# Performance work log

Hardware: AMD Instinct MI355X
Metric: run time of the kernel (lower is better)

The kernel has to match this reference:

```python
import jax, jax.numpy as jnp
import numpy as np

T_DIL = 10   # neighbor-count threshold
K_DIL = 2    # skip hyperparameter
BN_EPS = 1e-5
NORM_EPS = 1e-12


def _dilate_pattern(adj_bool, mask_b):
    """Sequential (row-by-row) dilated neighbor skipping on a [N,N] bool adjacency.
    Faithful to the torch double loop: earlier rows' removals (including the
    symmetric column zeroing) affect later rows' neighbor sets."""
    N = adj_bool.shape[0]

    def step(carry, n):
        row = jnp.take(carry, n, axis=0)                 # [N] bool, current neighbors of n
        nbi = row.astype(jnp.int32)
        num = jnp.sum(nbi)
        sf = jnp.where(num > T_DIL, (num + K_DIL - 1) // K_DIL, 1)  # linear mode, ceil(num/k)
        rank = jnp.cumsum(nbi)                           # 1-based rank among neighbors
        rm = row & ((rank % sf) == 0)                    # neighbors[sf-1::sf]
        valid = (mask_b[n] != 0) & (num > 1)
        rm = jnp.where(valid, rm, False)
        keep = ~rm
        carry = carry.at[n].set(row & keep)              # adj[n, to_remove] = 0
        carry = carry.at[:, n].set(carry[:, n] & keep)   # adj[to_remove, n] = 0
        return carry, None

    out, _ = jax.lax.scan(step, adj_bool, jnp.arange(N))
    return out


def _dilate(adj, mask):
    # keep-pattern is piecewise constant in adj; multiply so removed entries -> 0
    keep = jax.vmap(_dilate_pattern)(adj > 0, mask)
    return adj * keep.astype(adj.dtype)


def _sage(x, adj, Wr, Wx, b, mf):
    # DenseSAGEConv: mean-aggregate, lin_rel + lin_root, L2 normalize, mask
    deg = jnp.clip(jnp.sum(adj, axis=-1, keepdims=True), 1.0, None)
    agg = jnp.einsum('bij,bjd->bid', adj, x) / deg
    out = agg @ Wr + x @ Wx + b
    nrm = jnp.maximum(jnp.linalg.norm(out, axis=-1, keepdims=True), NORM_EPS)
    return (out / nrm) * mf[..., None]


def _bn(x, g, b):
    # BatchNorm1d in training mode over flattened (B*N) rows, biased variance
    m = jnp.mean(x, axis=(0, 1))
    v = jnp.var(x, axis=(0, 1))
    return (x - m) * jax.lax.rsqrt(v + BN_EPS) * g + b


def _forward(x, adj, mask, Wr1, Wx1, b1, g1, be1, Wr2, Wx2, b2, g2, be2,
             Wr3, Wx3, b3, g3, be3, Wl, bl):
    mf = mask.astype(x.dtype)
    # linear dilation mode: skip factor is layer-independent, and each layer
    # dilates the ORIGINAL adj (torch clones adj per call) -> compute once
    adj_d = _dilate(adj, mask)
    h1 = _bn(jax.nn.relu(_sage(x, adj_d, Wr1, Wx1, b1, mf)), g1, be1)
    h2 = _bn(jax.nn.relu(_sage(h1, adj_d, Wr2, Wx2, b2, mf)), g2, be2)
    h3 = _bn(jax.nn.relu(_sage(h2, adj_d, Wr3, Wx3, b3, mf)), g3, be3)
    xc = jnp.concatenate([h1, h2, h3], axis=-1) * mf[..., None]
    return (xc @ Wl + bl) * mf[..., None]


def setup_inputs() -> dict:
    B, N, D, H, E = 8, 2048, 128, 128, 128
    key = jax.random.key(0)
    ks = jax.random.split(key, 24)
    x = jax.random.normal(ks[0], (B, N, D), dtype=jnp.float32)
    a = jax.random.bernoulli(ks[1], 0.01, (B, N, N))
    a = a | jnp.swapaxes(a, 1, 2)
    a = a & ~jnp.eye(N, dtype=bool)[None]
    adj = a.astype(jnp.float32)
    mask = jnp.ones((B, N), dtype=jnp.int32)
    s = 0.05
    p = {}
    dims = [(D, H), (H, H), (H, E)]
    for i, (di, do) in enumerate(dims, 1):
        p[f'Wr{i}'] = s * jax.random.normal(ks[2 * i], (di, do), dtype=jnp.float32)
        p[f'Wx{i}'] = s * jax.random.normal(ks[2 * i + 1], (di, do), dtype=jnp.float32)
        p[f'b{i}'] = jnp.zeros((do,), dtype=jnp.float32)
        p[f'g{i}'] = jnp.ones((do,), dtype=jnp.float32)
        p[f'be{i}'] = jnp.zeros((do,), dtype=jnp.float32)
    p['Wl'] = s * jax.random.normal(ks[10], (2 * H + E, E), dtype=jnp.float32)
    p['bl'] = jnp.zeros((E,), dtype=jnp.float32)
    return {'x': x, 'adj': adj, 'mask': mask, **p}


def reference(x, adj, mask, Wr1, Wx1, b1, g1, be1, Wr2, Wx2, b2, g2, be2,
              Wr3, Wx3, b3, g3, be3, Wl, bl):
    return _forward(x, adj, mask, Wr1, Wx1, b1, g1, be1, Wr2, Wx2, b2, g2, be2,
                    Wr3, Wx3, b3, g3, be3, Wl, bl)
```

## Files before the change

kernel.cpp:

```cpp
#include <hip/hip_runtime.h>
#include <cstdint>

constexpr int B_ = 8, N_ = 2048, D_ = 128, NW = 64;
constexpr int EMAX = 131072;
constexpr int RPS = 2064;
constexpr int TDIL = 10;

constexpr size_t OFF_BITSET = 0;
constexpr size_t OFF_AGG    = 0;
constexpr size_t OFF_H1     = (size_t)8  << 20;
constexpr size_t OFF_H2     = (size_t)16 << 20;
constexpr size_t OFF_H3     = (size_t)24 << 20;
constexpr size_t OFF_XB     = (size_t)24 << 20;
constexpr size_t OFF_H1B    = (size_t)28 << 20;
constexpr size_t OFF_H2B    = (size_t)24 << 20;
constexpr size_t OFF_COLS   = (size_t)32 << 20;
constexpr size_t OFF_PACKED = (size_t)34 << 20;
constexpr size_t OFF_RP     = (size_t)38 << 20;
constexpr size_t OFF_DEG0   = OFF_RP   + ((size_t)128 << 10);
constexpr size_t OFF_DEGF   = OFF_DEG0 + ((size_t)64  << 10);
constexpr size_t OFF_RMASK  = OFF_DEGF + ((size_t)64  << 10);
constexpr size_t OFF_BN     = OFF_RMASK + ((size_t)256 << 10);
constexpr size_t OFF_WHI    = OFF_BN  + ((size_t)4 << 10);
constexpr size_t OFF_WLO    = OFF_WHI + ((size_t)304 << 10);

typedef __attribute__((ext_vector_type(8))) short short8v;
typedef __attribute__((ext_vector_type(4))) float f32x4;

__device__ __forceinline__ uint16_t bf16rne(float f) {
    uint32_t u = __float_as_uint(f);
    return (uint16_t)((u + 0x7FFFu + ((u >> 16) & 1u)) >> 16);
}

__global__ __launch_bounds__(256) void kW_prep(
        const float* __restrict__ Wr1, const float* __restrict__ Wx1,
        const float* __restrict__ Wr2, const float* __restrict__ Wx2,
        const float* __restrict__ Wr3, const float* __restrict__ Wx3,
        const float* __restrict__ Wl,
        uint16_t* __restrict__ whi, uint16_t* __restrict__ wlo,
        float* __restrict__ bn) {
    if (blockIdx.x == 0) {
        for (int i = threadIdx.x; i < 768; i += 256) bn[i] = 0.f;
    }
    int g  = blockIdx.x >> 5;
    int lb = blockIdx.x & 31;
    int K = (g == 3) ? 384 : 256;
    const float* A  = (g == 0) ? Wr1 : (g == 1) ? Wr2 : (g == 2) ? Wr3 : Wl;
    const float* Bw = (g == 0) ? Wx1 : (g == 1) ? Wx2 : (g == 2) ? Wx3 : nullptr;
    size_t base = (g == 3) ? (size_t)98304 : (size_t)g * 32768;
    int total = K * 128;
    for (int f = lb * 256 + threadIdx.x; f < total; f += 32 * 256) {
        int e = f & 7, lane = (f >> 3) & 63, ct = (f >> 9) & 7, ks = f >> 12;
        int k = ks * 32 + ((lane >> 4) << 3) + e;
        int col = (ct << 4) + (lane & 15);
        float v = (g == 3 || k < 128) ? A[(size_t)k * 128 + col]
                                      : Bw[(size_t)(k - 128) * 128 + col];
        uint32_t hi = bf16rne(v);
        float hf = __uint_as_float(hi << 16);
        whi[base + f] = (uint16_t)hi;
        wlo[base + f] = bf16rne(v - hf);
    }
}

__global__ __launch_bounds__(256) void kXB(const float* __restrict__ x,
                                           uint16_t* __restrict__ xb) {
    size_t i = ((size_t)blockIdx.x * 256 + threadIdx.x) * 4;
    float4 v = *(const float4*)&x[i];
    ushort4 o;
    o.x = bf16rne(v.x); o.y = bf16rne(v.y); o.z = bf16rne(v.z); o.w = bf16rne(v.w);
    *(ushort4*)&xb[i] = o;
}

__global__ __launch_bounds__(256) void k1_bitset(const float* __restrict__ adj,
        uint32_t* __restrict__ bitset, uint32_t* __restrict__ deg0) {
    int row  = blockIdx.x * 4 + (threadIdx.x >> 6);
    int lane = threadIdx.x & 63;
    const float* ar = adj + (size_t)row * N_;
    uint32_t myw = 0;
    #pragma unroll 4
    for (int it = 0; it < 32; ++it) {
        float v = ar[it * 64 + lane];
        unsigned long long m = __ballot(v != 0.0f);
        if (lane == 2 * it)          myw = (uint32_t)m;
        else if (lane == 2 * it + 1) myw = (uint32_t)(m >> 32);
    }
    bitset[(size_t)row * NW + lane] = myw;
    int pc = __popc(myw);
    #pragma unroll
    for (int off = 32; off >= 1; off >>= 1) pc += __shfl_xor(pc, off);
    if (lane == 0) deg0[row] = (uint32_t)pc;
}

__global__ __launch_bounds__(256) void k2_rowptr(const uint32_t* __restrict__ deg0,
        uint32_t* __restrict__ rowptr) {
    int b = blockIdx.x, t = threadIdx.x;
    __shared__ uint32_t tsum[256];
    uint32_t v[8]; uint32_t s = 0;
    #pragma unroll
    for (int j = 0; j < 8; ++j) { v[j] = deg0[b * N_ + t * 8 + j]; s += v[j]; v[j] = s; }
    tsum[t] = s;
    __syncthreads();
    for (int off = 1; off < 256; off <<= 1) {
        uint32_t xv = (t >= off) ? tsum[t - off] : 0u;
        __syncthreads();
        tsum[t] += xv;
        __syncthreads();
    }
    uint32_t excl = tsum[t] - s;
    uint32_t* rp = rowptr + (size_t)b * RPS;
    if (t == 0) rp[0] = 0;
    #pragma unroll
    for (int j = 0; j < 8; ++j) {
        uint32_t val = excl + v[j];
        if (val > (uint32_t)EMAX) val = EMAX;
        rp[t * 8 + j + 1] = val;
    }
}

__global__ __launch_bounds__(256) void k3_cols(const uint32_t* __restrict__ bitset,
        const uint32_t* __restrict__ rowptr, uint16_t* __restrict__ cols) {
    int row  = blockIdx.x * 4 + (threadIdx.x >> 6);
    int lane = threadIdx.x & 63;
    int b = row >> 11, n = row & (N_ - 1);
    uint32_t w = bitset[(size_t)row * NW + lane];
    uint32_t pc = __popc(w);
    uint32_t inc = pc;
    #pragma unroll
    for (int off = 1; off < 64; off <<= 1) {
        uint32_t t = __shfl_up(inc, off);
        if (lane >= off) inc += t;
    }
    uint32_t base = rowptr[(size_t)b * RPS + n] + (inc - pc);
    uint16_t* cb = cols + (size_t)b * EMAX;
    while (w) {
        int bit = __builtin_ctz(w); w &= w - 1;
        if (base < (uint32_t)EMAX) cb[base] = (uint16_t)(lane * 32 + bit);
        ++base;
    }
}

__global__ __launch_bounds__(256) void k4_packed(const uint16_t* __restrict__ cols,
        const uint32_t* __restrict__ rowptr, uint32_t* __restrict__ packed) {
    int row  = blockIdx.x * 4 + (threadIdx.x >> 6);
    int lane = threadIdx.x & 63;
    int b = row >> 11, n = row & (N_ - 1);
    const uint32_t* rpb = rowptr + (size_t)b * RPS;
    const uint16_t* cb  = cols + (size_t)b * EMAX;
    uint32_t start = rpb[n], end = rpb[n + 1];
    for (uint32_t e = start + lane; e < end; e += 64) {
        uint32_t j = cb[e];
        uint32_t lo = rpb[j], hi = rpb[j + 1];
        uint32_t rj = lo;
        while (lo < hi) {
            uint32_t mid = (lo + hi) >> 1;
            if ((int)cb[mid] < n) lo = mid + 1; else hi = mid;
        }
        packed[(size_t)b * EMAX + e] = j | ((lo - rj) << 16);
    }
}

#define K5_ISSUE(PK0, PK1, CNT, ROW)                                        \
    do {                                                                    \
        int rr_ = (ROW);                                                    \
        if (rr_ < N_) {                                                     \
            uint32_t ldI_ = rps[rr_], enI_ = rps[rr_ + 1];                  \
            CNT = (int)(enI_ - ldI_);                                       \
            PK0 = (lane < CNT)      ? pkg[ldI_ + lane]      : 0xFFFFFFFFu;  \
            PK1 = (lane + 64 < CNT) ? pkg[ldI_ + 64 + lane] : 0xFFFFFFFFu;  \
        } else { CNT = 0; PK0 = 0xFFFFFFFFu; PK1 = 0xFFFFFFFFu; }           \
    } while (0)

#define K5_PROC(PK0, PK1, CNT, NROW)                                        \
    do {                                                                    \
        int nr_ = (NROW);                                                   \
        uint32_t c0_ = PK0 & 0xFFFFu, c1_ = PK1 & 0xFFFFu;                  \
        bool e0_ = (lane < CNT)      && (c0_ < (uint32_t)nr_);              \
        bool e1_ = (lane + 64 < CNT) && (c1_ < (uint32_t)nr_);              \
        while (true) {                                                      \
            uint32_t d0_ = e0_ ? __hip_atomic_load(&done[c0_ >> 5],         \
                    __ATOMIC_ACQUIRE, __HIP_MEMORY_SCOPE_WORKGROUP) : 0u;   \
            uint32_t d1_ = e1_ ? __hip_atomic_load(&done[c1_ >> 5],         \
                    __ATOMIC_ACQUIRE, __HIP_MEMORY_SCOPE_WORKGROUP) : 0u;   \
            bool ok0_ = !e0_ || ((d0_ >> (c0_ & 31)) & 1u);                 \
            bool ok1_ = !e1_ || ((d1_ >> (c1_ & 31)) & 1u);                 \
            if (__all((int)(ok0_ && ok1_))) break;                          \
        }                                                                   \
        __builtin_amdgcn_s_setprio(1);                                      \
        uint4 mcur_ = *(const uint4*)&rm4[(size_t)nr_ * 4];                 \
        uint32_t w01_ = (lane < 32) ? mcur_.x : mcur_.y;                    \
        uint32_t w23_ = (lane < 32) ? mcur_.z : mcur_.w;                    \
        uint32_t a0_ = (w01_ >> (lane & 31)) & 1u;                          \
        uint32_t a1_ = (w23_ >> (lane & 31)) & 1u;                          \
        unsigned long long bl0_ = __ballot(a0_ != 0), bl1_ = __ballot(a1_ != 0); \
        uint32_t num_ = (uint32_t)__popcll(bl0_) + (uint32_t)__popcll(bl1_);\
        if (mk[nr_] && num_ > 1u) {                                         \
            bool allrm_ = num_ <= (uint32_t)TDIL;                           \
            uint32_t sf_ = (num_ + 1u) >> 1;                                \
            uint32_t r2_ = (num_ & 1u) ? 0xFFFFFFFFu : num_;                \
            uint32_t rank0_ = (uint32_t)__popcll(bl0_ & below) + 1u;        \
            uint32_t rank1_ = (uint32_t)__popcll(bl0_) +                    \
                              (uint32_t)__popcll(bl1_ & below) + 1u;        \
            bool rm0_ = a0_ && (allrm_ || rank0_ == sf_ || rank0_ == r2_);  \
            bool rm1_ = a1_ && (allrm_ || rank1_ == sf_ || rank1_ == r2_);  \
            unsigned long long rb0_ = __ballot(rm0_), rb1_ = __ballot(rm1_);\
            if (rm0_) {                                                     \
                uint32_t c_ = PK0 & 0xFFFFu, ml_ = PK0 >> 16;               \
                if (ml_ < 128u) atomicAnd(&rm4[c_ * 4 + (ml_ >> 5)], ~(1u << (ml_ & 31))); \
            }                                                               \
            if (rm1_) {                                                     \
                uint32_t c_ = PK1 & 0xFFFFu, ml_ = PK1 >> 16;               \
                if (ml_ < 128u) atomicAnd(&rm4[c_ * 4 + (ml_ >> 5)], ~(1u << (ml_ & 31))); \
            }                                                               \
            if (lane == 0) {                                                \
                uint4 nm_;                                                  \
                nm_.x = mcur_.x & ~(uint32_t)rb0_;                          \
                nm_.y = mcur_.y & ~(uint32_t)(rb0_ >> 32);                  \
                nm_.z = mcur_.z & ~(uint32_t)rb1_;                          \
                nm_.w = mcur_.w & ~(uint32_t)(rb1_ >> 32);                  \
                *(uint4*)&rm4[(size_t)nr_ * 4] = nm_;                       \
            }                                                               \
        }                                                                   \
        __asm__ __volatile__("" ::: "memory");                              \
        if (lane == 0)                                                      \
            __hip_atomic_fetch_or(&done[nr_ >> 5], 1u << (nr_ & 31),        \
                    __ATOMIC_RELAXED, __HIP_MEMORY_SCOPE_WORKGROUP);        \
        __builtin_amdgcn_s_setprio(0);                                      \
    } while (0)

__global__ __launch_bounds__(1024) void k5_dilate(
        const uint32_t* __restrict__ packed, const uint32_t* __restrict__ rowptr,
        const uint32_t* __restrict__ deg0, const int* __restrict__ mask,
        uint32_t* __restrict__ rmaskg, uint32_t* __restrict__ degf) {
    int b = blockIdx.x;
    int tid = threadIdx.x;
    int lane = tid & 63;
    int wv = tid >> 6;
    __shared__ __align__(16) uint32_t rm4[N_ * 4];
    __shared__ uint32_t rps[N_ + 1];
    __shared__ uint8_t  mk[N_];
    __shared__ uint32_t done[64];
    const uint32_t* pkg = packed + (size_t)b * EMAX;
    const uint32_t* rpg = rowptr + (size_t)b * RPS;

    for (int i = tid; i <= N_; i += 1024) rps[i] = rpg[i];
    if (tid < 64) done[tid] = 0u;
    for (int i = tid; i < N_; i += 1024) {
        int d = (int)deg0[b * N_ + i]; if (d > 128) d = 128;
        uint4 mm;
        mm.x = (d >= 32) ? ~0u : ((d > 0)  ? ((1u << d)        - 1u) : 0u);
        mm.y = (d >= 64) ? ~0u : ((d > 32) ? ((1u << (d - 32)) - 1u) : 0u);
        mm.z = (d >= 96) ? ~0u : ((d > 64) ? ((1u << (d - 64)) - 1u) : 0u);
        mm.w = (d >= 128)? ~0u : ((d > 96) ? ((1u << (d - 96)) - 1u) : 0u);
        *(uint4*)&rm4[(size_t)i * 4] = mm;
        mk[i] = (uint8_t)(mask[b * N_ + i] != 0);
    }
    __syncthreads();

    unsigned long long below = (1ULL << lane) - 1ULL;
    int cntA, cntB, cntC;
    uint32_t pkA0, pkA1, pkB0, pkB1, pkC0, pkC1;
    K5_ISSUE(pkA0, pkA1, cntA, wv);
    K5_ISSUE(pkB0, pkB1, cntB, wv + 16);
    K5_ISSUE(pkC0, pkC1, cntC, wv + 32);

    int n = wv;
    while (n < N_) {
        K5_PROC(pkA0, pkA1, cntA, n);
        K5_ISSUE(pkA0, pkA1, cntA, n + 48);
        n += 16; if (n >= N_) break;
        K5_PROC(pkB0, pkB1, cntB, n);
        K5_ISSUE(pkB0, pkB1, cntB, n + 48);
        n += 16; if (n >= N_) break;
        K5_PROC(pkC0, pkC1, cntC, n);
        K5_ISSUE(pkC0, pkC1, cntC, n + 48);
        n += 16;
    }
    __syncthreads();
    for (int i = tid; i < N_; i += 1024) {
        uint4 mm = *(const uint4*)&rm4[(size_t)i * 4];
        *(uint4*)&rmaskg[((size_t)b * N_ + i) * 4] = mm;
        degf[b * N_ + i] = (uint32_t)(__popc(mm.x) + __popc(mm.y) + __popc(mm.z) + __popc(mm.w));
    }
}

__global__ __launch_bounds__(256) void k6_compact(uint16_t* __restrict__ cols,
        const uint32_t* __restrict__ rowptr, const uint32_t* __restrict__ rmaskg) {
    int row  = blockIdx.x * 4 + (threadIdx.x >> 6);
    int lane = threadIdx.x & 63;
    int b = row >> 11, n = row & (N_ - 1);
    uint16_t* cb = cols + (size_t)b * EMAX;
    uint4 mm = *(const uint4*)&rmaskg[(size_t)row * 4];
    uint32_t st = rowptr[(size_t)b * RPS + n];
    uint32_t w01 = (lane < 32) ? mm.x : mm.y;
    uint32_t w23 = (lane < 32) ? mm.z : mm.w;
    uint32_t a0 = (w01 >> (lane & 31)) & 1u;
    uint32_t a1 = (w23 >> (lane & 31)) & 1u;
    unsigned long long b0 = __ballot(a0 != 0), b1 = __ballot(a1 != 0);
    unsigned long long below = (1ULL << lane) - 1ULL;
    uint16_t c0v = 0, c1v = 0;
    if (a0) c0v = cb[st + lane];
    if (a1) c1v = cb[st + 64 + lane];
    uint32_t i0 = st + (uint32_t)__popcll(b0 & below);
    uint32_t i1 = st + (uint32_t)__popcll(b0) + (uint32_t)__popcll(b1 & below);
    if (a0) cb[i0] = c0v;
    if (a1) cb[i1] = c1v;
}

__global__ __launch_bounds__(256) void k7_spmm(const uint16_t* __restrict__ Xb16,
        const uint16_t* __restrict__ cols, const uint32_t* __restrict__ rowptr,
        const uint32_t* __restrict__ degf, float* __restrict__ agg) {
    int wid  = blockIdx.x * 4 + (threadIdx.x >> 6);
    int lane = threadIdx.x & 63;
    int b = wid >> 11, n = wid & (N_ - 1);
    const uint16_t* cb = cols + (size_t)b * EMAX;
    uint32_t start = rowptr[(size_t)b * RPS + n];
    uint32_t cnt = degf[wid];
    const uint16_t* Xb = Xb16 + ((size_t)b * N_) * D_;
    float ax = 0.f, ay = 0.f;
    for (uint32_t base = 0; base < cnt; base += 64) {
        int idx = (int)base + lane;
        int cl = (idx < (int)cnt) ? (int)cb[start + idx] : 0;
        int kmax = (int)cnt - (int)base; if (kmax > 64) kmax = 64;
        int k = 0;
        for (; k + 4 <= kmax; k += 4) {
            int cA = __shfl(cl, k),     cB = __shfl(cl, k + 1);
            int cC = __shfl(cl, k + 2), cD = __shfl(cl, k + 3);
            uint32_t uA = ((const uint32_t*)(Xb + (size_t)cA * D_))[lane];
            uint32_t uB = ((const uint32_t*)(Xb + (size_t)cB * D_))[lane];
            uint32_t uC = ((const uint32_t*)(Xb + (size_t)cC * D_))[lane];
            uint32_t uD = ((const uint32_t*)(Xb + (size_t)cD * D_))[lane];
            ax += __uint_as_float(uA << 16) + __uint_as_float(uB << 16)
                + __uint_as_float(uC << 16) + __uint_as_float(uD << 16);
            ay += __uint_as_float(uA & 0xFFFF0000u) + __uint_as_float(uB & 0xFFFF0000u)
                + __uint_as_float(uC & 0xFFFF0000u) + __uint_as_float(uD & 0xFFFF0000u);
        }
        for (; k < kmax; ++k) {
            int c = __shfl(cl, k);
            uint32_t u = ((const uint32_t*)(Xb + (size_t)c * D_))[lane];
            ax += __uint_as_float(u << 16);
            ay += __uint_as_float(u & 0xFFFF0000u);
        }
    }
    float inv = 1.0f / (float)(cnt ? cnt : 1u);
    ((float2*)(agg + (size_t)wid * D_))[lane] = make_float2(ax * inv, ay * inv);
}

__device__ __forceinline__ void cvt_store4(uint16_t* hiA, uint16_t* loA,
                                           int idx, float4 v) {
    float vv[4] = {v.x, v.y, v.z, v.w};
    ushort4 hs, ls;
    uint16_t* hp = (uint16_t*)&hs; uint16_t* lp = (uint16_t*)&ls;
    #pragma unroll
    for (int i = 0; i < 4; ++i) {
        uint32_t hi = bf16rne(vv[i]);
        float hf = __uint_as_float(hi << 16);
        hp[i] = (uint16_t)hi;
        lp[i] = bf16rne(vv[i] - hf);
    }
    *(ushort4*)&hiA[idx] = hs;
    *(ushort4*)&loA[idx] = ls;
}

constexpr int ASTR = 264;
__global__ __launch_bounds__(256) void k8_mfma(const float* __restrict__ agg,
        const float* __restrict__ Hin,
        const uint16_t* __restrict__ whi, const uint16_t* __restrict__ wlo,
        const float* __restrict__ bias, const int* __restrict__ mask,
        const float* __restrict__ bnp, const float* __restrict__ gp,
        const float* __restrict__ bep, int use_bn,
        float* __restrict__ P, uint16_t* __restrict__ Pb,
        float* __restrict__ bnstat) {
    __shared__ __align__(16) char buf[2 * 32 * ASTR * 2];
    __shared__ float scL[128], shL[128];
    uint16_t* aHi = (uint16_t*)buf;
    uint16_t* aLo = (uint16_t*)(buf + 32 * ASTR * 2);
    float* outP = (float*)buf;
    int tid = threadIdx.x, lane = tid & 63, h = tid >> 6;
    size_t row0 = (size_t)blockIdx.x * 32;

    if (tid < 128) {
        float sc = 1.f, sh = 0.f;
        if (use_bn) {
            float mean = bnp[tid] * (1.f / 16384.f);
            float var  = bnp[128 + tid] * (1.f / 16384.f) - mean * mean;
            sc = gp[tid] * rsqrtf(var + 1e-5f);
            sh = bep[tid] - mean * sc;
        }
        scL[tid] = sc; shL[tid] = sh;
    }
    __syncthreads();

    for (int f = tid * 4; f < 4096; f += 1024) {
        int r = f >> 7, c = f & 127;
        float4 va = *(const float4*)&agg[(row0 + r) * 128 + c];
        float4 vx = *(const float4*)&Hin[(row0 + r) * 128 + c];
        float4 s4 = *(const float4*)&scL[c];
        float4 h4 = *(const float4*)&shL[c];
        va.x = va.x * s4.x + h4.x; va.y = va.y * s4.y + h4.y;
        va.z = va.z * s4.z + h4.z; va.w = va.w * s4.w + h4.w;
        vx.x = vx.x * s4.x + h4.x; vx.y = vx.y * s4.y + h4.y;
        vx.z = vx.z * s4.z + h4.z; vx.w = vx.w * s4.w + h4.w;
        cvt_store4(aHi, aLo, r * ASTR + c, va);
        cvt_store4(aHi, aLo, r * ASTR + 128 + c, vx);
    }
    __syncthreads();

    f32x4 acc00 = {0.f,0.f,0.f,0.f}, acc01 = acc00, acc10 = acc00, acc11 = acc00;
    int ct0 = h * 2, ct1 = h * 2 + 1;
    int arow = (lane & 15);
    int koff = (lane >> 4) * 8;
    #pragma unroll
    for (int ks = 0; ks < 8; ++ks) {
        int k0 = ks * 32 + koff;
        short8v a0h = *(short8v*)&aHi[arow * ASTR + k0];
        short8v a0l = *(short8v*)&aLo[arow * ASTR + k0];
        short8v a1h = *(short8v*)&aHi[(arow + 16) * ASTR + k0];
        short8v a1l = *(short8v*)&aLo[(arow + 16) * ASTR + k0];
        short8v b0h = *(const short8v*)&whi[(size_t)(((ks * 8 + ct0) << 6) + lane) * 8];
        short8v b0l = *(const short8v*)&wlo[(size_t)(((ks * 8 + ct0) << 6) + lane) * 8];
        short8v b1h = *(const short8v*)&whi[(size_t)(((ks * 8 + ct1) << 6) + lane) * 8];
        short8v b1l = *(const short8v*)&wlo[(size_t)(((ks * 8 + ct1) << 6) + lane) * 8];
        acc00 = __builtin_amdgcn_mfma_f32_16x16x32_bf16(a0h, b0h, acc00, 0, 0, 0);
        acc00 = __builtin_amdgcn_mfma_f32_16x16x32_bf16(a0h, b0l, acc00, 0, 0, 0);
        acc00 = __builtin_amdgcn_mfma_f32_16x16x32_bf16(a0l, b0h, acc00, 0, 0, 0);
        acc01 = __builtin_amdgcn_mfma_f32_16x16x32_bf16(a0h, b1h, acc01, 0, 0, 0);
        acc01 = __builtin_amdgcn_mfma_f32_16x16x32_bf16(a0h, b1l, acc01, 0, 0, 0);
        acc01 = __builtin_amdgcn_mfma_f32_16x16x32_bf16(a0l, b1h, acc01, 0, 0, 0);
        acc10 = __builtin_amdgcn_mfma_f32_16x16x32_bf16(a1h, b0h, acc10, 0, 0, 0);
        acc10 = __builtin_amdgcn_mfma_f32_16x16x32_bf16(a1h, b0l, acc10, 0, 0, 0);
        acc10 = __builtin_amdgcn_mfma_f32_16x16x32_bf16(a1l, b0h, acc10, 0, 0, 0);
        acc11 = __builtin_amdgcn_mfma_f32_16x16x32_bf16(a1h, b1h, acc11, 0, 0, 0);
        acc11 = __builtin_amdgcn_mfma_f32_16x16x32_bf16(a1h, b1l, acc11, 0, 0, 0);
        acc11 = __builtin_amdgcn_mfma_f32_16x16x32_bf16(a1l, b1h, acc11, 0, 0, 0);
    }
    __syncthreads();

    int orow = (lane >> 4) * 4;
    int oc0 = ct0 * 16 + (lane & 15);
    int oc1 = ct1 * 16 + (lane & 15);
    #pragma unroll
    for (int j = 0; j < 4; ++j) {
        outP[(orow + j) * 128 + oc0]      = acc00[j];
        outP[(orow + j) * 128 + oc1]      = acc01[j];
        outP[(16 + orow + j) * 128 + oc0] = acc10[j];
        outP[(16 + orow + j) * 128 + oc1] = acc11[j];
    }
    __syncthreads();

    float bs0 = bias[lane], bs1 = bias[lane + 64];
    #pragma unroll
    for (int i = 0; i < 8; ++i) {
        int r = h * 8 + i;
        float v0 = outP[r * 128 + lane] + bs0;
        float v1 = outP[r * 128 + lane + 64] + bs1;
        float s = v0 * v0 + v1 * v1;
        #pragma unroll
        for (int off = 32; off >= 1; off >>= 1) s += __shfl_xor(s, off);
        float nrm = fmaxf(sqrtf(s), 1e-12f);
        float mf = (mask[row0 + r] != 0) ? 1.f : 0.f;
        float inv = mf / nrm;
        float p0 = fmaxf(v0 * inv, 0.f), p1 = fmaxf(v1 * inv, 0.f);
        P[(row0 + r) * 128 + lane]      = p0;
        P[(row0 + r) * 128 + lane + 64] = p1;
        if (Pb) {
            Pb[(row0 + r) * 128 + lane]      = bf16rne(p0);
            Pb[(row0 + r) * 128 + lane + 64] = bf16rne(p1);
        }
        outP[r * 128 + lane] = p0; outP[r * 128 + lane + 64] = p1;
    }
    __syncthreads();
    if (tid < 128) {
        float s = 0.f, q = 0.f;
        #pragma unroll
        for (int r = 0; r < 32; ++r) { float v = outP[r * 128 + tid]; s += v; q += v * v; }
        atomicAdd(&bnstat[tid], s);
        atomicAdd(&bnstat[128 + tid], q);
    }
}

__global__ __launch_bounds__(256) void k11_final(const float* __restrict__ h1,
        const float* __restrict__ h2, const float* __restrict__ h3,
        const float* __restrict__ Wl, const float* __restrict__ bl,
        const int* __restrict__ mask, const float* __restrict__ bn,
        const float* __restrict__ g1, const float* __restrict__ be1,
        const float* __restrict__ g2, const float* __restrict__ be2,
        const float* __restrict__ g3, const float* __restrict__ be3,
        float* __restrict__ out) {
    __shared__ float s1[32 * 128], s2[32 * 128], s3[32 * 128];
    __shared__ float scA[128], shA[128], scB[128], shB[128], scC[128], shC[128];
    int tid = threadIdx.x;
    size_t row0 = (size_t)blockIdx.x * 32;
    if (tid < 128) {
        float m1 = bn[tid] * (1.f / 16384.f);
        float v1 = bn[128 + tid] * (1.f / 16384.f) - m1 * m1;
        scA[tid] = g1[tid] * rsqrtf(v1 + 1e-5f);
        shA[tid] = be1[tid] - m1 * scA[tid];
        float m2 = bn[256 + tid] * (1.f / 16384.f);
        float v2 = bn[384 + tid] * (1.f / 16384.f) - m2 * m2;
        scB[tid] = g2[tid] * rsqrtf(v2 + 1e-5f);
        shB[tid] = be2[tid] - m2 * scB[tid];
        float m3 = bn[512 + tid] * (1.f / 16384.f);
        float v3 = bn[640 + tid] * (1.f / 16384.f) - m3 * m3;
        scC[tid] = g3[tid] * rsqrtf(v3 + 1e-5f);
        shC[tid] = be3[tid] - m3 * scC[tid];
    }
    __syncthreads();
    for (int t = tid * 4; t < 32 * 128; t += 1024) {
        int r = t >> 7;
        float mf = (mask[row0 + r] != 0) ? 1.f : 0.f;
        int c = t & 127;
        float4 a = *(const float4*)&h1[row0 * 128 + t];
        float4 b = *(const float4*)&h2[row0 * 128 + t];
        float4 cc = *(const float4*)&h3[row0 * 128 + t];
        float4 sa = *(const float4*)&scA[c], ha = *(const float4*)&shA[c];
        float4 sb = *(const float4*)&scB[c], hb = *(const float4*)&shB[c];
        float4 sc = *(const float4*)&scC[c], hc = *(const float4*)&shC[c];
        a.x = (a.x * sa.x + ha.x) * mf; a.y = (a.y * sa.y + ha.y) * mf;
        a.z = (a.z * sa.z + ha.z) * mf; a.w = (a.w * sa.w + ha.w) * mf;
        b.x = (b.x * sb.x + hb.x) * mf; b.y = (b.y * sb.y + hb.y) * mf;
        b.z = (b.z * sb.z + hb.z) * mf; b.w = (b.w * sb.w + hb.w) * mf;
        cc.x = (cc.x * sc.x + hc.x) * mf; cc.y = (cc.y * sc.y + hc.y) * mf;
        cc.z = (cc.z * sc.z + hc.z) * mf; cc.w = (cc.w * sc.w + hc.w) * mf;
        *(float4*)&s1[t] = a; *(float4*)&s2[t] = b; *(float4*)&s3[t] = cc;
    }
    __syncthreads();
    int h = tid >> 6, c0 = (tid & 63) * 2;
    float2 acc[8];
    #pragma unroll
    for (int i = 0; i < 8; ++i) acc[i] = make_float2(0.f, 0.f);
    for (int k4 = 0; k4 < 128; k4 += 4) {
        float2 w1[4], w2[4], w3[4];
        #pragma unroll
        for (int kk = 0; kk < 4; ++kk) {
            w1[kk] = *(const float2*)&Wl[(k4 + kk) * 128 + c0];
            w2[kk] = *(const float2*)&Wl[(128 + k4 + kk) * 128 + c0];
            w3[kk] = *(const float2*)&Wl[(256 + k4 + kk) * 128 + c0];
        }
        #pragma unroll
        for (int i = 0; i < 8; ++i) {
            int r = h * 8 + i;
            float4 a = *(const float4*)&s1[r * 128 + k4];
            float4 b = *(const float4*)&s2[r * 128 + k4];
            float4 c = *(const float4*)&s3[r * 128 + k4];
            acc[i].x += a.x * w1[0].x + a.y * w1[1].x + a.z * w1[2].x + a.w * w1[3].x
                      + b.x * w2[0].x + b.y * w2[1].x + b.z * w2[2].x + b.w * w2[3].x
                      + c.x * w3[0].x + c.y * w3[1].x + c.z * w3[2].x + c.w * w3[3].x;
            acc[i].y += a.x * w1[0].y + a.y * w1[1].y + a.z * w1[2].y + a.w * w1[3].y
                      + b.x * w2[0].y + b.y * w2[1].y + b.z * w2[2].y + b.w * w2[3].y
                      + c.x * w3[0].y + c.y * w3[1].y + c.z * w3[2].y + c.w * w3[3].y;
        }
    }
    float bx = bl[c0], by = bl[c0 + 1];
    #pragma unroll
    for (int i = 0; i < 8; ++i) {
        int r = h * 8 + i;
        float mf = (mask[row0 + r] != 0) ? 1.f : 0.f;
        *(float2*)&out[(row0 + r) * 128 + c0] =
            make_float2((acc[i].x + bx) * mf, (acc[i].y + by) * mf);
    }
}

extern "C" void kernel_launch(void* const* d_in, const int* in_sizes, int n_in,
                              void* d_out, int out_size, void* d_ws, size_t ws_size,
                              hipStream_t stream) {
    (void)in_sizes; (void)n_in; (void)out_size; (void)ws_size;
    const float* x    = (const float*)d_in[0];
    const float* adj  = (const float*)d_in[1];
    const int*   mask = (const int*)d_in[2];
    const float* Wr1 = (const float*)d_in[3],  *Wx1 = (const float*)d_in[4];
    const float* b1  = (const float*)d_in[5],  *g1  = (const float*)d_in[6],  *be1 = (const float*)d_in[7];
    const float* Wr2 = (const float*)d_in[8],  *Wx2 = (const float*)d_in[9];
    const float* b2  = (const float*)d_in[10], *g2  = (const float*)d_in[11], *be2 = (const float*)d_in[12];
    const float* Wr3 = (const float*)d_in[13], *Wx3 = (const float*)d_in[14];
    const float* b3  = (const float*)d_in[15], *g3  = (const float*)d_in[16], *be3 = (const float*)d_in[17];
    const float* Wl  = (const float*)d_in[18], *bl  = (const float*)d_in[19];

    char* ws = (char*)d_ws;
    uint32_t* bitset = (uint32_t*)(ws + OFF_BITSET);
    float*    agg    = (float*)(ws + OFF_AGG);
    float*    h1     = (float*)(ws + OFF_H1);
    float*    h2     = (float*)(ws + OFF_H2);
    float*    h3     = (float*)(ws + OFF_H3);
    uint16_t* xb     = (uint16_t*)(ws + OFF_XB);
    uint16_t* h1b    = (uint16_t*)(ws + OFF_H1B);
    uint16_t* h2b    = (uint16_t*)(ws + OFF_H2B);
    uint16_t* cols   = (uint16_t*)(ws + OFF_COLS);
    uint32_t* packed = (uint32_t*)(ws + OFF_PACKED);
    uint32_t* rp     = (uint32_t*)(ws + OFF_RP);
    uint32_t* deg0   = (uint32_t*)(ws + OFF_DEG0);
    uint32_t* degf   = (uint32_t*)(ws + OFF_DEGF);
    uint32_t* rmaskg = (uint32_t*)(ws + OFF_RMASK);
    float*    bn     = (float*)(ws + OFF_BN);
    uint16_t* whi    = (uint16_t*)(ws + OFF_WHI);
    uint16_t* wlo    = (uint16_t*)(ws + OFF_WLO);
    float*    out    = (float*)d_out;

    kW_prep   <<<128,  256, 0, stream>>>(Wr1, Wx1, Wr2, Wx2, Wr3, Wx3, Wl, whi, wlo, bn);
    kXB       <<<2048, 256, 0, stream>>>(x, xb);
    k1_bitset <<<4096, 256, 0, stream>>>(adj, bitset, deg0);
    k2_rowptr <<<8,    256, 0, stream>>>(deg0, rp);
    k3_cols   <<<4096, 256, 0, stream>>>(bitset, rp, cols);
    k4_packed <<<4096, 256, 0, stream>>>(cols, rp, packed);
    k5_dilate <<<8,    1024, 0, stream>>>(packed, rp, deg0, mask, rmaskg, degf);
    k6_compact<<<4096, 256, 0, stream>>>(cols, rp, rmaskg);
    k7_spmm   <<<4096, 256, 0, stream>>>(xb,  cols, rp, degf, agg);
    k8_mfma   <<<512,  256, 0, stream>>>(agg, x,  whi,         wlo,         b1, mask,
                                         bn, g1, be1, 0, h1, h1b, bn + 0);
    k7_spmm   <<<4096, 256, 0, stream>>>(h1b, cols, rp, degf, agg);
    k8_mfma   <<<512,  256, 0, stream>>>(agg, h1, whi + 32768, wlo + 32768, b2, mask,
                                         bn + 0, g1, be1, 1, h2, h2b, bn + 256);
    k7_spmm   <<<4096, 256, 0, stream>>>(h2b, cols, rp, degf, agg);
    k8_mfma   <<<512,  256, 0, stream>>>(agg, h2, whi + 65536, wlo + 65536, b3, mask,
                                         bn + 256, g2, be2, 1, h3, nullptr, bn + 512);
    k11_final <<<512,  256, 0, stream>>>(h1, h2, h3, Wl, bl, mask, bn,
                                         g1, be1, g2, be2, g3, be3, out);
}
```

Measured before the change: 313.9 us.

## Fuse compaction into dilation kernel, merge bf16 cast into weight prep, add single-wave fast path

Folds the x-to-bf16 conversion into the weight-prep launch as extra blocks, and moves the per-row column compaction into the tail of the dilation kernel, reading the mask from shared memory. This removes two launches and the global round trip of the row-removal mask. It also adds a fast path in the sequential dilation loop for rows with at most 64 neighbors, which skips the second half's loads, polls and ballots. The trade-off is that compaction now runs on only 8 blocks instead of 4096, so it has much less parallelism.

```diff
diff --git a/kernel.cpp b/kernel.cpp
--- a/kernel.cpp
+++ b/kernel.cpp
@@ -19,8 +19,7 @@
 constexpr size_t OFF_RP     = (size_t)38 << 20;
 constexpr size_t OFF_DEG0   = OFF_RP   + ((size_t)128 << 10);
 constexpr size_t OFF_DEGF   = OFF_DEG0 + ((size_t)64  << 10);
-constexpr size_t OFF_RMASK  = OFF_DEGF + ((size_t)64  << 10);
-constexpr size_t OFF_BN     = OFF_RMASK + ((size_t)256 << 10);
+constexpr size_t OFF_BN     = OFF_DEGF + ((size_t)64  << 10);
 constexpr size_t OFF_WHI    = OFF_BN  + ((size_t)4 << 10);
 constexpr size_t OFF_WLO    = OFF_WHI + ((size_t)304 << 10);
 
@@ -38,7 +37,17 @@
         const float* __restrict__ Wr3, const float* __restrict__ Wx3,
         const float* __restrict__ Wl,
         uint16_t* __restrict__ whi, uint16_t* __restrict__ wlo,
-        float* __restrict__ bn) {
+        float* __restrict__ bn,
+        const float* __restrict__ x, uint16_t* __restrict__ xb) {
+    if (blockIdx.x >= 128) {
+        size_t i = ((size_t)(blockIdx.x - 128) * 256 + threadIdx.x) * 4;
+        float4 v = *(const float4*)&x[i];
+        ushort4 o;
+        o.x = bf16rne(v.x); o.y = bf16rne(v.y);
+        o.z = bf16rne(v.z); o.w = bf16rne(v.w);
+        *(ushort4*)&xb[i] = o;
+        return;
+    }
     if (blockIdx.x == 0) {
         for (int i = threadIdx.x; i < 768; i += 256) bn[i] = 0.f;
     }
@@ -62,15 +71,6 @@
     }
 }
 
-__global__ __launch_bounds__(256) void kXB(const float* __restrict__ x,
-                                           uint16_t* __restrict__ xb) {
-    size_t i = ((size_t)blockIdx.x * 256 + threadIdx.x) * 4;
-    float4 v = *(const float4*)&x[i];
-    ushort4 o;
-    o.x = bf16rne(v.x); o.y = bf16rne(v.y); o.z = bf16rne(v.z); o.w = bf16rne(v.w);
-    *(ushort4*)&xb[i] = o;
-}
-
 __global__ __launch_bounds__(256) void k1_bitset(const float* __restrict__ adj,
         uint32_t* __restrict__ bitset, uint32_t* __restrict__ deg0) {
     int row  = blockIdx.x * 4 + (threadIdx.x >> 6);
@@ -165,72 +165,116 @@
         if (rr_ < N_) {                                                     \
             uint32_t ldI_ = rps[rr_], enI_ = rps[rr_ + 1];                  \
             CNT = (int)(enI_ - ldI_);                                       \
-            PK0 = (lane < CNT)      ? pkg[ldI_ + lane]      : 0xFFFFFFFFu;  \
-            PK1 = (lane + 64 < CNT) ? pkg[ldI_ + 64 + lane] : 0xFFFFFFFFu;  \
+            PK0 = (lane < CNT) ? pkg[ldI_ + lane] : 0xFFFFFFFFu;            \
+            if (CNT > 64)                                                   \
+                PK1 = (lane + 64 < CNT) ? pkg[ldI_ + 64 + lane] : 0xFFFFFFFFu; \
+            else PK1 = 0xFFFFFFFFu;                                         \
         } else { CNT = 0; PK0 = 0xFFFFFFFFu; PK1 = 0xFFFFFFFFu; }           \
     } while (0)
 
 #define K5_PROC(PK0, PK1, CNT, NROW)                                        \
     do {                                                                    \
         int nr_ = (NROW);                                                   \
-        uint32_t c0_ = PK0 & 0xFFFFu, c1_ = PK1 & 0xFFFFu;                  \
-        bool e0_ = (lane < CNT)      && (c0_ < (uint32_t)nr_);              \
-        bool e1_ = (lane + 64 < CNT) && (c1_ < (uint32_t)nr_);              \
-        while (true) {                                                      \
-            uint32_t d0_ = e0_ ? __hip_atomic_load(&done[c0_ >> 5],         \
-                    __ATOMIC_ACQUIRE, __HIP_MEMORY_SCOPE_WORKGROUP) : 0u;   \
-            uint32_t d1_ = e1_ ? __hip_atomic_load(&done[c1_ >> 5],         \
-                    __ATOMIC_ACQUIRE, __HIP_MEMORY_SCOPE_WORKGROUP) : 0u;   \
-            bool ok0_ = !e0_ || ((d0_ >> (c0_ & 31)) & 1u);                 \
-            bool ok1_ = !e1_ || ((d1_ >> (c1_ & 31)) & 1u);                 \
-            if (__all((int)(ok0_ && ok1_))) break;                          \
+        if (CNT <= 64) {                                                    \
+                            \
+            uint32_t c0_ = PK0 & 0xFFFFu;                                   \
+            bool e0_ = (lane < CNT) && (c0_ < (uint32_t)nr_);               \
+            while (true) {                                                  \
+                uint32_t d0_ = e0_ ? __hip_atomic_load(&done[c0_ >> 5],     \
+                        __ATOMIC_ACQUIRE, __HIP_MEMORY_SCOPE_WORKGROUP) : 0u; \
+                bool ok0_ = !e0_ || ((d0_ >> (c0_ & 31)) & 1u);             \
+                if (__all((int)ok0_)) break;                                \
+            }                                                               \
+            __builtin_amdgcn_s_setprio(1);                                  \
+            uint2 mc_ = *(const uint2*)&rm4[(size_t)nr_ * 4];               \
+            uint32_t w01_ = (lane < 32) ? mc_.x : mc_.y;                    \
+            uint32_t a0_ = (w01_ >> (lane & 31)) & 1u;                      \
+            unsigned long long bl0_ = __ballot(a0_ != 0);                   \
+            uint32_t num_ = (uint32_t)__popcll(bl0_);                       \
+            if (mk[nr_] && num_ > 1u) {                                     \
+                bool allrm_ = num_ <= (uint32_t)TDIL;                       \
+                uint32_t sf_ = (num_ + 1u) >> 1;                            \
+                uint32_t r2_ = (num_ & 1u) ? 0xFFFFFFFFu : num_;            \
+                uint32_t rank0_ = (uint32_t)__popcll(bl0_ & below) + 1u;    \
+                bool rm0_ = a0_ && (allrm_ || rank0_ == sf_ || rank0_ == r2_); \
+                unsigned long long rb0_ = __ballot(rm0_);                   \
+                if (rm0_) {                                                 \
+                    uint32_t ml_ = PK0 >> 16;                               \
+                    if (ml_ < 128u) atomicAnd(&rm4[c0_ * 4 + (ml_ >> 5)], ~(1u << (ml_ & 31))); \
+                }                                                           \
+                if (lane == 0) {                                            \
+                    uint2 nm_;                                              \
+                    nm_.x = mc_.x & ~(uint32_t)rb0_;                        \
+                    nm_.y = mc_.y & ~(uint32_t)(rb0_ >> 32);                \
+                    *(uint2*)&rm4[(size_t)nr_ * 4] = nm_;                   \
+                }                                                           \
+            }                                                               \
+            __asm__ __volatile__("" ::: "memory");                          \
+            if (lane == 0)                                                  \
+                __hip_atomic_fetch_or(&done[nr_ >> 5], 1u << (nr_ & 31),    \
+                        __ATOMIC_RELAXED, __HIP_MEMORY_SCOPE_WORKGROUP);    \
+            __builtin_amdgcn_s_setprio(0);                                  \
+        } else {                                                            \
+                      \
+            uint32_t c0_ = PK0 & 0xFFFFu, c1_ = PK1 & 0xFFFFu;              \
+            bool e0_ = (lane < CNT)      && (c0_ < (uint32_t)nr_);          \
+            bool e1_ = (lane + 64 < CNT) && (c1_ < (uint32_t)nr_);          \
+            while (true) {                                                  \
+                uint32_t d0_ = e0_ ? __hip_atomic_load(&done[c0_ >> 5],     \
+                        __ATOMIC_ACQUIRE, __HIP_MEMORY_SCOPE_WORKGROUP) : 0u; \
+                uint32_t d1_ = e1_ ? __hip_atomic_load(&done[c1_ >> 5],     \
+                        __ATOMIC_ACQUIRE, __HIP_MEMORY_SCOPE_WORKGROUP) : 0u; \
+                bool ok0_ = !e0_ || ((d0_ >> (c0_ & 31)) & 1u);             \
+                bool ok1_ = !e1_ || ((d1_ >> (c1_ & 31)) & 1u);             \
+                if (__all((int)(ok0_ && ok1_))) break;                      \
+            }                                                               \
+            __builtin_amdgcn_s_setprio(1);                                  \
+            uint4 mcur_ = *(const uint4*)&rm4[(size_t)nr_ * 4];             \
+            uint32_t w01_ = (lane < 32) ? mcur_.x : mcur_.y;                \
+            uint32_t w23_ = (lane < 32) ? mcur_.z : mcur_.w;                \
+            uint32_t a0_ = (w01_ >> (lane & 31)) & 1u;                      \
+            uint32_t a1_ = (w23_ >> (lane & 31)) & 1u;                      \
+            unsigned long long bl0_ = __ballot(a0_ != 0), bl1_ = __ballot(a1_ != 0); \
+            uint32_t num_ = (uint32_t)__popcll(bl0_) + (uint32_t)__popcll(bl1_); \
+            if (mk[nr_] && num_ > 1u) {                                     \
+                bool allrm_ = num_ <= (uint32_t)TDIL;                       \
+                uint32_t sf_ = (num_ + 1u) >> 1;                            \
+                uint32_t r2_ = (num_ & 1u) ? 0xFFFFFFFFu : num_;            \
+                uint32_t rank0_ = (uint32_t)__popcll(bl0_ & below) + 1u;    \
+                uint32_t rank1_ = (uint32_t)__popcll(bl0_) +                \
+                                  (uint32_t)__popcll(bl1_ & below) + 1u;    \
+                bool rm0_ = a0_ && (allrm_ || rank0_ == sf_ || rank0_ == r2_); \
+                bool rm1_ = a1_ && (allrm_ || rank1_ == sf_ || rank1_ == r2_); \
+                unsigned long long rb0_ = __ballot(rm0_), rb1_ = __ballot(rm1_); \
+                if (rm0_) {                                                 \
+                    uint32_t ml_ = PK0 >> 16;                               \
+                    if (ml_ < 128u) atomicAnd(&rm4[c0_ * 4 + (ml_ >> 5)], ~(1u << (ml_ & 31))); \
+                }                                                           \
+                if (rm1_) {                                                 \
+                    uint32_t ml_ = PK1 >> 16;                               \
+                    if (ml_ < 128u) atomicAnd(&rm4[c1_ * 4 + (ml_ >> 5)], ~(1u << (ml_ & 31))); \
+                }                                                           \
+                if (lane == 0) {                                            \
+                    uint4 nm_;                                              \
+                    nm_.x = mcur_.x & ~(uint32_t)rb0_;                      \
+                    nm_.y = mcur_.y & ~(uint32_t)(rb0_ >> 32);              \
+                    nm_.z = mcur_.z & ~(uint32_t)rb1_;                      \
+                    nm_.w = mcur_.w & ~(uint32_t)(rb1_ >> 32);              \
+                    *(uint4*)&rm4[(size_t)nr_ * 4] = nm_;                   \
+                }                                                           \
+            }                                                               \
+            __asm__ __volatile__("" ::: "memory");                          \
+            if (lane == 0)                                                  \
+                __hip_atomic_fetch_or(&done[nr_ >> 5], 1u << (nr_ & 31),    \
+                        __ATOMIC_RELAXED, __HIP_MEMORY_SCOPE_WORKGROUP);    \
+            __builtin_amdgcn_s_setprio(0);                                  \
         }                                                                   \
-        __builtin_amdgcn_s_setprio(1);                                      \
-        uint4 mcur_ = *(const uint4*)&rm4[(size_t)nr_ * 4];                 \
-        uint32_t w01_ = (lane < 32) ? mcur_.x : mcur_.y;                    \
-        uint32_t w23_ = (lane < 32) ? mcur_.z : mcur_.w;                    \
-        uint32_t a0_ = (w01_ >> (lane & 31)) & 1u;                          \
-        uint32_t a1_ = (w23_ >> (lane & 31)) & 1u;                          \
-        unsigned long long bl0_ = __ballot(a0_ != 0), bl1_ = __ballot(a1_ != 0); \
-        uint32_t num_ = (uint32_t)__popcll(bl0_) + (uint32_t)__popcll(bl1_);\
-        if (mk[nr_] && num_ > 1u) {                                         \
-            bool allrm_ = num_ <= (uint32_t)TDIL;                           \
-            uint32_t sf_ = (num_ + 1u) >> 1;                                \
-            uint32_t r2_ = (num_ & 1u) ? 0xFFFFFFFFu : num_;                \
-            uint32_t rank0_ = (uint32_t)__popcll(bl0_ & below) + 1u;        \
-            uint32_t rank1_ = (uint32_t)__popcll(bl0_) +                    \
-                              (uint32_t)__popcll(bl1_ & below) + 1u;        \
-            bool rm0_ = a0_ && (allrm_ || rank0_ == sf_ || rank0_ == r2_);  \
-            bool rm1_ = a1_ && (allrm_ || rank1_ == sf_ || rank1_ == r2_);  \
-            unsigned long long rb0_ = __ballot(rm0_), rb1_ = __ballot(rm1_);\
-            if (rm0_) {                                                     \
-                uint32_t c_ = PK0 & 0xFFFFu, ml_ = PK0 >> 16;               \
-                if (ml_ < 128u) atomicAnd(&rm4[c_ * 4 + (ml_ >> 5)], ~(1u << (ml_ & 31))); \
-            }                                                               \
-            if (rm1_) {                                                     \
-                uint32_t c_ = PK1 & 0xFFFFu, ml_ = PK1 >> 16;               \
-                if (ml_ < 128u) atomicAnd(&rm4[c_ * 4 + (ml_ >> 5)], ~(1u << (ml_ & 31))); \
-            }                                                               \
-            if (lane == 0) {                                                \
-                uint4 nm_;                                                  \
-                nm_.x = mcur_.x & ~(uint32_t)rb0_;                          \
-                nm_.y = mcur_.y & ~(uint32_t)(rb0_ >> 32);                  \
-                nm_.z = mcur_.z & ~(uint32_t)rb1_;                          \
-                nm_.w = mcur_.w & ~(uint32_t)(rb1_ >> 32);                  \
-                *(uint4*)&rm4[(size_t)nr_ * 4] = nm_;                       \
-            }                                                               \
-        }                                                                   \
-        __asm__ __volatile__("" ::: "memory");                              \
-        if (lane == 0)                                                      \
-            __hip_atomic_fetch_or(&done[nr_ >> 5], 1u << (nr_ & 31),        \
-                    __ATOMIC_RELAXED, __HIP_MEMORY_SCOPE_WORKGROUP);        \
-        __builtin_amdgcn_s_setprio(0);                                      \
     } while (0)
 
-__global__ __launch_bounds__(1024) void k5_dilate(
+__global__ __launch_bounds__(1024) void k5_fused(
         const uint32_t* __restrict__ packed, const uint32_t* __restrict__ rowptr,
         const uint32_t* __restrict__ deg0, const int* __restrict__ mask,
-        uint32_t* __restrict__ rmaskg, uint32_t* __restrict__ degf) {
+        uint16_t* __restrict__ cols, uint32_t* __restrict__ degf) {
     int b = blockIdx.x;
     int tid = threadIdx.x;
     int lane = tid & 63;
@@ -241,6 +285,7 @@
     __shared__ uint32_t done[64];
     const uint32_t* pkg = packed + (size_t)b * EMAX;
     const uint32_t* rpg = rowptr + (size_t)b * RPS;
+    uint16_t* cbm = cols + (size_t)b * EMAX;
 
     for (int i = tid; i <= N_; i += 1024) rps[i] = rpg[i];
     if (tid < 64) done[tid] = 0u;
@@ -276,34 +321,26 @@
         n += 16;
     }
     __syncthreads();
-    for (int i = tid; i < N_; i += 1024) {
+
+    for (int i = wv; i < N_; i += 16) {
         uint4 mm = *(const uint4*)&rm4[(size_t)i * 4];
-        *(uint4*)&rmaskg[((size_t)b * N_ + i) * 4] = mm;
-        degf[b * N_ + i] = (uint32_t)(__popc(mm.x) + __popc(mm.y) + __popc(mm.z) + __popc(mm.w));
-    }
-}
-
-__global__ __launch_bounds__(256) void k6_compact(uint16_t* __restrict__ cols,
-        const uint32_t* __restrict__ rowptr, const uint32_t* __restrict__ rmaskg) {
-    int row  = blockIdx.x * 4 + (threadIdx.x >> 6);
-    int lane = threadIdx.x & 63;
-    int b = row >> 11, n = row & (N_ - 1);
-    uint16_t* cb = cols + (size_t)b * EMAX;
-    uint4 mm = *(const uint4*)&rmaskg[(size_t)row * 4];
-    uint32_t st = rowptr[(size_t)b * RPS + n];
-    uint32_t w01 = (lane < 32) ? mm.x : mm.y;
-    uint32_t w23 = (lane < 32) ? mm.z : mm.w;
-    uint32_t a0 = (w01 >> (lane & 31)) & 1u;
-    uint32_t a1 = (w23 >> (lane & 31)) & 1u;
-    unsigned long long b0 = __ballot(a0 != 0), b1 = __ballot(a1 != 0);
-    unsigned long long below = (1ULL << lane) - 1ULL;
-    uint16_t c0v = 0, c1v = 0;
-    if (a0) c0v = cb[st + lane];
-    if (a1) c1v = cb[st + 64 + lane];
-    uint32_t i0 = st + (uint32_t)__popcll(b0 & below);
-    uint32_t i1 = st + (uint32_t)__popcll(b0) + (uint32_t)__popcll(b1 & below);
-    if (a0) cb[i0] = c0v;
-    if (a1) cb[i1] = c1v;
+        if (lane == 0)
+            degf[b * N_ + i] = (uint32_t)(__popc(mm.x) + __popc(mm.y) +
+                                          __popc(mm.z) + __popc(mm.w));
+        uint32_t st = rps[i];
+        uint32_t w01 = (lane < 32) ? mm.x : mm.y;
+        uint32_t w23 = (lane < 32) ? mm.z : mm.w;
+        uint32_t a0 = (w01 >> (lane & 31)) & 1u;
+        uint32_t a1 = (w23 >> (lane & 31)) & 1u;
+        unsigned long long b0 = __ballot(a0 != 0), b1v = __ballot(a1 != 0);
+        uint16_t c0v = 0, c1v = 0;
+        if (a0) c0v = cbm[st + lane];
+        if (a1) c1v = cbm[st + 64 + lane];
+        uint32_t i0 = st + (uint32_t)__popcll(b0 & below);
+        uint32_t i1 = st + (uint32_t)__popcll(b0) + (uint32_t)__popcll(b1v & below);
+        if (a0) cbm[i0] = c0v;
+        if (a1) cbm[i1] = c1v;
+    }
 }
 
 __global__ __launch_bounds__(256) void k7_spmm(const uint16_t* __restrict__ Xb16,
@@ -589,20 +626,18 @@
     uint32_t* rp     = (uint32_t*)(ws + OFF_RP);
     uint32_t* deg0   = (uint32_t*)(ws + OFF_DEG0);
     uint32_t* degf   = (uint32_t*)(ws + OFF_DEGF);
-    uint32_t* rmaskg = (uint32_t*)(ws + OFF_RMASK);
     float*    bn     = (float*)(ws + OFF_BN);
     uint16_t* whi    = (uint16_t*)(ws + OFF_WHI);
     uint16_t* wlo    = (uint16_t*)(ws + OFF_WLO);
     float*    out    = (float*)d_out;
 
-    kW_prep   <<<128,  256, 0, stream>>>(Wr1, Wx1, Wr2, Wx2, Wr3, Wx3, Wl, whi, wlo, bn);
-    kXB       <<<2048, 256, 0, stream>>>(x, xb);
+    kW_prep   <<<2176, 256, 0, stream>>>(Wr1, Wx1, Wr2, Wx2, Wr3, Wx3, Wl,
+                                         whi, wlo, bn, x, xb);
     k1_bitset <<<4096, 256, 0, stream>>>(adj, bitset, deg0);
     k2_rowptr <<<8,    256, 0, stream>>>(deg0, rp);
     k3_cols   <<<4096, 256, 0, stream>>>(bitset, rp, cols);
     k4_packed <<<4096, 256, 0, stream>>>(cols, rp, packed);
-    k5_dilate <<<8,    1024, 0, stream>>>(packed, rp, deg0, mask, rmaskg, degf);
-    k6_compact<<<4096, 256, 0, stream>>>(cols, rp, rmaskg);
+    k5_fused  <<<8,    1024, 0, stream>>>(packed, rp, deg0, mask, cols, degf);
     k7_spmm   <<<4096, 256, 0, stream>>>(xb,  cols, rp, degf, agg);
     k8_mfma   <<<512,  256, 0, stream>>>(agg, x,  whi,         wlo,         b1, mask,
                                          bn, g1, be1, 0, h1, h1b, bn + 0);
```

Result: slower. 330.3 us (+5.2%).
